# Optimization experiments

Measured on AMD Instinct MI355X. Metric: run time of the kernel, lower is better.

Reference implementation:

```python
import jax, jax.numpy as jnp
import numpy as np

N, G = 10000, 200          # nodes, graphs
EL, EG = 160000, 500000    # local / global edges
S, V = 256, 64             # scalar / vector hidden dims
NA, NB = 16, 5             # atom types, bond types


def _lin(k, i, o):
    return (jax.random.normal(k, (i, o), jnp.float32) / np.sqrt(i))


def scatter_mean(vals, idx, num_segments):
    # vals: [N, ...]; idx: [N] int
    sums = jax.ops.segment_sum(vals, idx, num_segments=num_segments)
    cnt = jax.ops.segment_sum(jnp.ones((vals.shape[0],), vals.dtype), idx,
                              num_segments=num_segments)
    cnt = jnp.maximum(cnt, 1.0).reshape((-1,) + (1,) * (vals.ndim - 1))
    return sums / cnt


def calc_edge_attrs(edge_index, pos):
    src, tgt = edge_index[0], edge_index[1]
    r = pos[tgt] - pos[src]                      # [E,3]
    a = (pos[tgt] * pos[src]).sum(-1)            # [E]
    d = jnp.sqrt(jnp.clip((r ** 2).sum(-1), 1e-6))
    r_norm = r / d[:, None]
    return d, a, r_norm


def setup_inputs() -> dict:
    key = jax.random.key(0)
    ks = jax.random.split(key, 24)
    inp = {}
    inp["x"] = jax.random.normal(ks[0], (N, NA), jnp.float32)
    inp["t"] = jax.random.uniform(ks[1], (G, 1), jnp.float32)
    inp["pos"] = jax.random.normal(ks[2], (N, 3), jnp.float32)
    eil = jax.random.randint(ks[3], (2, EL), 0, N)
    eig = jax.random.randint(ks[4], (2, EG), 0, N)
    # avoid self-edges so edge distances are strictly positive (safe sqrt grads)
    eig = eig.at[1].set(jnp.where(eig[1] == eig[0], (eig[1] + 1) % N, eig[1]))
    eil = eil.at[1].set(jnp.where(eil[1] == eil[0], (eil[1] + 1) % N, eil[1]))
    inp["edge_index_local"] = eil
    inp["edge_index_global"] = eig
    inp["edge_attr_global"] = jax.random.normal(ks[5], (EG, NB), jnp.float32)
    inp["batch"] = jnp.sort(jax.random.randint(ks[6], (N,), 0, G))
    # learned parameters
    inp["W_time"], inp["b_time"] = _lin(ks[7], 1, S), jnp.zeros((S,), jnp.float32)
    inp["W_atom"], inp["b_atom"] = _lin(ks[8], NA, S), jnp.zeros((S,), jnp.float32)
    inp["W_at"], inp["b_at"] = _lin(ks[9], S, S), jnp.zeros((S,), jnp.float32)
    inp["W_shared"], inp["b_shared"] = _lin(ks[10], S, S), jnp.zeros((S,), jnp.float32)
    inp["W_b0"], inp["b_b0"] = _lin(ks[11], S + 1, S), jnp.zeros((S,), jnp.float32)
    inp["W_b1"], inp["b_b1"] = _lin(ks[12], S, 2 * NB), jnp.zeros((2 * NB,), jnp.float32)
    inp["W_coord"] = _lin(ks[13], V, 2)           # no bias
    inp["W_atoms"], inp["b_atoms"] = _lin(ks[14], S, 2 * NA), jnp.zeros((2 * NA,), jnp.float32)
    return inp


def reference(x, t, pos, edge_attr_global, W_time, b_time, W_atom, b_atom,
              W_at, b_at, W_shared, b_shared, W_b0, b_b0, W_b1, b_b1,
              W_coord, W_atoms, b_atoms,
              edge_index_local, edge_index_global, batch):
    # --- trunk: center positions, embed atoms + time ---
    pos = pos - scatter_mean(pos, batch, G)[batch]
    temb = t @ W_time + b_time                    # [G,S]
    tnode = temb[batch]                           # [N,S]
    s = x @ W_atom + b_atom
    s = (s + tnode) @ W_at + b_at                 # [N,S]
    # --- edge attrs (gather-compute pattern feeding the GNN) ---
    d_l, a_l, rn_l = calc_edge_attrs(edge_index_local, pos)
    d_g, a_g, rn_g = calc_edge_attrs(edge_index_global, pos)
    # GNN stand-in (identity on s, v, p): v initialized to zeros as in original
    v = jnp.zeros((N, 3, V), s.dtype)
    # --- prediction head ---
    s = jax.nn.silu(s @ W_shared + b_shared)
    j, i = edge_index_global[0], edge_index_global[1]
    d = jnp.sqrt(((pos[i] - pos[j]) ** 2).sum(-1, keepdims=True))  # [EG,1]
    edge = jnp.concatenate([s[i] + s[j], d], axis=-1)              # [EG,S+1]
    bonds = jax.nn.silu(edge @ W_b0 + b_b0) @ W_b1 + b_b1          # [EG,2*NB]
    bonds_pred, bonds_eps = bonds[:, :NB], bonds[:, NB:]
    coords = jnp.einsum('nkv,vo->nko', v, W_coord)                 # [N,3,2]
    coords = coords - scatter_mean(coords, batch, G)[batch]
    coords_eps0, coords_eps1 = coords[..., 0], coords[..., 1]      # [N,3]
    atoms = s @ W_atoms + b_atoms                                  # [N,2*NA]
    atoms_eps, atoms_pred = atoms[:, :NA], atoms[:, NA:]
    pos_c = pos - scatter_mean(pos, batch, G)[batch]
    coords_pred = pos_c + coords_eps1
    return (coords_pred, coords_eps0, atoms_pred, atoms_eps,
            bonds_pred, bonds_eps, d_l, rn_l, a_g, rn_g)
```

## Files before the change

kernel.cpp:

```cpp
#include <hip/hip_runtime.h>
#include <hip/hip_bf16.h>

typedef __hip_bfloat16 bf16;
typedef short bf16x8 __attribute__((ext_vector_type(8)));
typedef float f32x4 __attribute__((ext_vector_type(4)));
typedef float f32x2 __attribute__((ext_vector_type(2)));
typedef _Float16 f16x2 __attribute__((ext_vector_type(2)));
typedef _Float16 f16x8 __attribute__((ext_vector_type(8)));
typedef __fp16 fp16x2 __attribute__((ext_vector_type(2)));

#define N_NODES  10000
#define G_GRAPHS 200
#define EL_EDGES 160000
#define EG_EDGES 500000
#define S_DIM    256
#define APAD     264

#define BONDS2        7813
#define LOCAL_BLOCKS  625

#define WS_FLAG   0
#define WS_POSC   1024
#define WS_WDH    31232
#define WS_W1F    31488
#define WS_BB0R   33536
#define WS_BB1    34304
#define WS_WATOM  34560
#define WS_WTIME  38656
#define WS_BTIME  38912
#define WS_BATOM  39168
#define WS_BAT    39424
#define WS_BSH    39680
#define WS_BATOMS 39936
#define WS_T      40000
#define WS_X      40448
#define WT_AT     200448
#define WT_SH     233216
#define WT_B0     265984
#define WT_ATOMS  298752
#define WS_H      303968
#define WS_END_FLOATS 944224

#define CHAN(S)    ((((S) >> 6) << 6) + (((S) & 3) << 4) + (((S) & 63) >> 2))

#define O_CPRED 0
#define O_CEPS  30000
#define O_APRED 60000
#define O_AEPS  220000
#define O_BPRED 380000
#define O_BEPS  2880000
#define O_DL    5380000
#define O_RNL   5540000
#define O_AG    6020000
#define O_RNG   6520000

__device__ __forceinline__ float b2f(bf16 v) { return __bfloat162float(v); }
__device__ __forceinline__ bf16  f2b(float v) { return __float2bfloat16(v); }
__device__ __forceinline__ unsigned short bbits(float v) {
    bf16 b = f2b(v);
    return *reinterpret_cast<unsigned short*>(&b);
}
__device__ __forceinline__ unsigned short h16bits(float v) {
    _Float16 h = (_Float16)v;
    return *reinterpret_cast<unsigned short*>(&h);
}
__device__ __forceinline__ float ldin(const void* p, int idx, int isf32) {
    return isf32 ? ((const float*)p)[idx] : b2f(((const bf16*)p)[idx]);
}
__device__ __forceinline__ void stout(void* out, int f32o, size_t idx, float v) {
    if (f32o) ((float*)out)[idx] = v;
    else      ((bf16*)out)[idx]  = f2b(v);
}
__device__ __forceinline__ float silu(float p) {
    return p * __builtin_amdgcn_rcpf(1.0f + __expf(-p));
}
__device__ __forceinline__ _Float16 h_exp2(_Float16 x) {
    _Float16 r;
    asm("v_exp_f16 %0, %1" : "=v"(r) : "v"(x));
    return r;
}
__device__ __forceinline__ _Float16 h_rcp(_Float16 x) {
    _Float16 r;
    asm("v_rcp_f16 %0, %1" : "=v"(r) : "v"(x));
    return r;
}
__device__ __forceinline__ f16x2 hsilu2(f16x2 p) {
    const _Float16 nl = (_Float16)(-1.44269504f);
    f16x2 q = p * (f16x2){nl, nl};
    f16x2 ex;
    ex[0] = h_exp2(q[0]);
    ex[1] = h_exp2(q[1]);
    f16x2 den = ex + (f16x2){(_Float16)1.0f, (_Float16)1.0f};
    f16x2 rc;
    rc[0] = h_rcp(den[0]);
    rc[1] = h_rcp(den[1]);
    return p * rc;
}
template<bool HI>
__device__ __forceinline__ f16x2 dec2(int enc) {
    f32x2 f = __builtin_amdgcn_cvt_pk_f32_fp8(enc, HI);
    union { fp16x2 a; f16x2 b; } u;
    u.a = __builtin_amdgcn_cvt_pkrtz(f[0], f[1]);
    return u.b;
}
__device__ __forceinline__ int dtype_f32(const void* tt) {
    const unsigned short* q = (const unsigned short*)tt;
    int c = 0;
#pragma unroll
    for (int z = 0; z < 32; ++z) c += (q[z] >= 0x4000) ? 1 : 0;
    return c > 0;
}

__global__ void k_prep(const void* __restrict__ x, const void* __restrict__ tt,
                       const void* __restrict__ W_time, const void* __restrict__ b_time,
                       const void* __restrict__ W_atom, const void* __restrict__ b_atom,
                       const void* __restrict__ W_at, const void* __restrict__ b_at,
                       const void* __restrict__ W_shared, const void* __restrict__ b_shared,
                       const void* __restrict__ W_b0, const void* __restrict__ b_b0,
                       const void* __restrict__ W_b1, const void* __restrict__ b_b1,
                       const void* __restrict__ W_atoms, const void* __restrict__ b_atoms,
                       float* __restrict__ ws) {
    const int t = blockIdx.x * blockDim.x + threadIdx.x;
    const int f = dtype_f32(tt);
    if (t == 0) ws[WS_FLAG] = f ? 1.0f : 0.0f;
    if (t < 65536) {
        const int k = t >> 8, n = t & 255;
        ((unsigned short*)(ws + WT_AT))[n * 256 + k] = bbits(ldin(W_at, t, f));
        ((unsigned short*)(ws + WT_SH))[n * 256 + k] = bbits(ldin(W_shared, t, f));
        ((unsigned short*)(ws + WT_B0))[n * 256 + k] = bbits(ldin(W_b0, t, f));
    }
    if (t < 160000) ws[WS_X + t] = ldin(x, t, f);
    if (t < 8192) {
        const int k = t >> 5, n = t & 31;
        ((unsigned short*)(ws + WT_ATOMS))[n * 256 + k] = bbits(ldin(W_atoms, t, f));
    }
    if (t < 4096) {
        const int i = t & 7, lc = (t >> 3) & 15, q = (t >> 7) & 3, ts = t >> 9;
        const int s = ts * 32 + q * 8 + i;
        float v = (lc < 10) ? ldin(W_b1, CHAN(s) * 10 + lc, f) : 0.0f;
        ((unsigned short*)(ws + WS_W1F))[t] = h16bits(v);
    }
    if (t < 4096) ws[WS_WATOM + t] = ldin(W_atom, t, f);
    if (t < 256) {
        ((unsigned short*)(ws + WS_WDH))[t] = h16bits(ldin(W_b0, 65536 + CHAN(t), f));
        ws[WS_BB0R + t] = ldin(b_b0, t, f);
        ws[WS_WTIME + t] = ldin(W_time, t, f);
        ws[WS_BTIME + t] = ldin(b_time, t, f);
        ws[WS_BATOM + t] = ldin(b_atom, t, f);
        ws[WS_BAT + t]   = ldin(b_at, t, f);
        ws[WS_BSH + t]   = ldin(b_shared, t, f);
    }
    if (t < 200) ws[WS_T + t] = ldin(tt, t, f);
    if (t < 32)  ws[WS_BATOMS + t] = ldin(b_atoms, t, f);
    if (t < 16)  ws[WS_BB1 + t] = (t < 10) ? ldin(b_b1, t, f) : 0.0f;
}

__global__ void k_pos(const void* __restrict__ pos, const int* __restrict__ batch,
                      float* __restrict__ ws, void* __restrict__ out) {
    const int g = blockIdx.x;
    const int f32o = ws[WS_FLAG] != 0.0f;
    __shared__ int s_lo, s_hi;
    __shared__ float wsum[4][3];
    __shared__ float mean[3];
    if (threadIdx.x == 0) {
        int lo = 0, hi = N_NODES;
        while (lo < hi) { int m = (lo + hi) >> 1; if (batch[m] < g) lo = m + 1; else hi = m; }
        s_lo = lo;
        int lo2 = lo; hi = N_NODES;
        while (lo2 < hi) { int m = (lo2 + hi) >> 1; if (batch[m] < g + 1) lo2 = m + 1; else hi = m; }
        s_hi = lo2;
    }
    __syncthreads();
    const int lo = s_lo, hi = s_hi, cnt = hi - lo;
    float sx = 0.f, sy = 0.f, sz = 0.f;
    for (int n = lo + threadIdx.x; n < hi; n += 256) {
        sx += ldin(pos, n * 3 + 0, f32o);
        sy += ldin(pos, n * 3 + 1, f32o);
        sz += ldin(pos, n * 3 + 2, f32o);
    }
#pragma unroll
    for (int off = 32; off > 0; off >>= 1) {
        sx += __shfl_down(sx, off);
        sy += __shfl_down(sy, off);
        sz += __shfl_down(sz, off);
    }
    if ((threadIdx.x & 63) == 0) {
        wsum[threadIdx.x >> 6][0] = sx;
        wsum[threadIdx.x >> 6][1] = sy;
        wsum[threadIdx.x >> 6][2] = sz;
    }
    __syncthreads();
    if (threadIdx.x == 0) {
        float inv = 1.0f / (float)max(cnt, 1);
        mean[0] = (wsum[0][0] + wsum[1][0] + wsum[2][0] + wsum[3][0]) * inv;
        mean[1] = (wsum[0][1] + wsum[1][1] + wsum[2][1] + wsum[3][1]) * inv;
        mean[2] = (wsum[0][2] + wsum[1][2] + wsum[2][2] + wsum[3][2]) * inv;
    }
    __syncthreads();
    for (int n = lo + threadIdx.x; n < hi; n += 256) {
#pragma unroll
        for (int k = 0; k < 3; ++k) {
            float p = ldin(pos, n * 3 + k, f32o) - mean[k];
            ws[WS_POSC + n * 3 + k] = p;
            stout(out, f32o, O_CPRED + n * 3 + k, p);
            stout(out, f32o, O_CEPS + n * 3 + k, 0.0f);
        }
    }
}

__global__ __launch_bounds__(256) void k_node(
    const int* __restrict__ batch, const float* __restrict__ ws,
    unsigned int* __restrict__ h_out, void* __restrict__ out) {
    __shared__ unsigned short actA[16][APAD];
    __shared__ unsigned short actB[16][APAD];
    const int tid = threadIdx.x;
    const int wave = tid >> 6, lane = tid & 63;
    const int quad = lane >> 4, l16 = lane & 15;
    const int row0 = blockIdx.x * 16;

    {
        const int r = tid >> 4;
        const int c0 = (tid & 15) * 16;
        const int g = row0 + r;
        float tb = ws[WS_T + batch[g]];
        float xr[16];
#pragma unroll
        for (int k = 0; k < 16; ++k) xr[k] = ws[WS_X + g * 16 + k];
        for (int cc = 0; cc < 16; cc += 4) {
            const int c = c0 + cc;
            float a0 = ws[WS_BATOM + c + 0] + tb * ws[WS_WTIME + c + 0] + ws[WS_BTIME + c + 0];
            float a1 = ws[WS_BATOM + c + 1] + tb * ws[WS_WTIME + c + 1] + ws[WS_BTIME + c + 1];
            float a2 = ws[WS_BATOM + c + 2] + tb * ws[WS_WTIME + c + 2] + ws[WS_BTIME + c + 2];
            float a3 = ws[WS_BATOM + c + 3] + tb * ws[WS_WTIME + c + 3] + ws[WS_BTIME + c + 3];
#pragma unroll
            for (int k = 0; k < 16; ++k) {
                float4 w4 = *(const float4*)(ws + WS_WATOM + k * S_DIM + c);
                a0 += xr[k] * w4.x; a1 += xr[k] * w4.y;
                a2 += xr[k] * w4.z; a3 += xr[k] * w4.w;
            }
            actA[r][c + 0] = bbits(a0); actA[r][c + 1] = bbits(a1);
            actA[r][c + 2] = bbits(a2); actA[r][c + 3] = bbits(a3);
        }
    }
    __syncthreads();

    const unsigned short* wt_at = (const unsigned short*)(ws + WT_AT);
    const unsigned short* wt_sh = (const unsigned short*)(ws + WT_SH);
    const unsigned short* wt_b0 = (const unsigned short*)(ws + WT_B0);
    const unsigned short* wt_am = (const unsigned short*)(ws + WT_ATOMS);
    const int n0 = wave * 64;

    {
        f32x4 acc[4] = {};
        for (int kk = 0; kk < S_DIM; kk += 32) {
            const int k = kk + quad * 8;
            bf16x8 a = *(const bf16x8*)&actA[l16][k];
#pragma unroll
            for (int nt = 0; nt < 4; ++nt) {
                bf16x8 b = *(const bf16x8*)(wt_at + (size_t)(n0 + nt * 16 + l16) * S_DIM + k);
                acc[nt] = __builtin_amdgcn_mfma_f32_16x16x32_bf16(a, b, acc[nt], 0, 0, 0);
            }
        }
#pragma unroll
        for (int nt = 0; nt < 4; ++nt) {
            const int n = n0 + nt * 16 + l16;
            const float bv = ws[WS_BAT + n];
#pragma unroll
            for (int r = 0; r < 4; ++r)
                actB[quad * 4 + r][n] = bbits(acc[nt][r] + bv);
        }
    }
    __syncthreads();

    {
        f32x4 acc[4] = {};
        for (int kk = 0; kk < S_DIM; kk += 32) {
            const int k = kk + quad * 8;
            bf16x8 a = *(const bf16x8*)&actB[l16][k];
#pragma unroll
            for (int nt = 0; nt < 4; ++nt) {
                bf16x8 b = *(const bf16x8*)(wt_sh + (size_t)(n0 + nt * 16 + l16) * S_DIM + k);
                acc[nt] = __builtin_amdgcn_mfma_f32_16x16x32_bf16(a, b, acc[nt], 0, 0, 0);
            }
        }
        __syncthreads();
#pragma unroll
        for (int nt = 0; nt < 4; ++nt) {
            const int n = n0 + nt * 16 + l16;
            const float bv = ws[WS_BSH + n];
#pragma unroll
            for (int r = 0; r < 4; ++r)
                actA[quad * 4 + r][n] = bbits(silu(acc[nt][r] + bv));
        }
    }
    __syncthreads();

    {
        f32x4 acc[4] = {};
        for (int kk = 0; kk < S_DIM; kk += 32) {
            const int k = kk + quad * 8;
            bf16x8 a = *(const bf16x8*)&actA[l16][k];
#pragma unroll
            for (int nt = 0; nt < 4; ++nt) {
                bf16x8 b = *(const bf16x8*)(wt_b0 + (size_t)(n0 + nt * 16 + l16) * S_DIM + k);
                acc[nt] = __builtin_amdgcn_mfma_f32_16x16x32_bf16(a, b, acc[nt], 0, 0, 0);
            }
        }
        float bh[4];
#pragma unroll
        for (int nt = 0; nt < 4; ++nt) bh[nt] = 0.5f * ws[WS_BB0R + n0 + nt * 16 + l16];
#pragma unroll
        for (int r = 0; r < 4; ++r) {
            const int g = row0 + quad * 4 + r;
            int w = 0;
            w = __builtin_amdgcn_cvt_pk_fp8_f32(acc[0][r] + bh[0], acc[1][r] + bh[1], w, false);
            w = __builtin_amdgcn_cvt_pk_fp8_f32(acc[2][r] + bh[2], acc[3][r] + bh[3], w, true);
            h_out[(size_t)g * 64 + wave * 16 + l16] = (unsigned int)w;
        }
    }

    if (wave < 2) {
        f32x4 acc = {};
        const int n = wave * 16 + l16;
        for (int kk = 0; kk < S_DIM; kk += 32) {
            const int k = kk + quad * 8;
            bf16x8 a = *(const bf16x8*)&actA[l16][k];
            bf16x8 b = *(const bf16x8*)(wt_am + (size_t)n * S_DIM + k);
            acc = __builtin_amdgcn_mfma_f32_16x16x32_bf16(a, b, acc, 0, 0, 0);
        }
        const float bv = ws[WS_BATOMS + n];
        const int f32o = ws[WS_FLAG] != 0.0f;
#pragma unroll
        for (int r = 0; r < 4; ++r) {
            const int g = row0 + quad * 4 + r;
            float v = acc[r] + bv;
            if (n < 16) stout(out, f32o, O_AEPS + (size_t)g * 16 + n, v);
            else        stout(out, f32o, O_APRED + (size_t)g * 16 + (n - 16), v);
        }
    }
}

union U8 { f16x8 v; f16x2 p[4]; };

__global__ __launch_bounds__(256, 4) void k_edges(const int* __restrict__ eig,
                                                  const int* __restrict__ eil,
                                                  const float* __restrict__ ws,
                                                  const unsigned char* __restrict__ h,
                                                  void* __restrict__ out) {
    __shared__ unsigned char sm[4][32][256];
    const int f32o = ws[WS_FLAG] != 0.0f;

    if (blockIdx.x >= BONDS2) {
        const int e = (blockIdx.x - BONDS2) * 256 + threadIdx.x;
        const float* posc = ws + WS_POSC;
        const int s = eil[e];
        const int t = eil[EL_EDGES + e];
        float rx = posc[t * 3 + 0] - posc[s * 3 + 0];
        float ry = posc[t * 3 + 1] - posc[s * 3 + 1];
        float rz = posc[t * 3 + 2] - posc[s * 3 + 2];
        float dsq = rx * rx + ry * ry + rz * rz;
        float d = sqrtf(fmaxf(dsq, 1e-6f));
        float inv = 1.0f / d;
        stout(out, f32o, O_DL + e, d);
        stout(out, f32o, O_RNL + (size_t)e * 3 + 0, rx * inv);
        stout(out, f32o, O_RNL + (size_t)e * 3 + 1, ry * inv);
        stout(out, f32o, O_RNL + (size_t)e * 3 + 2, rz * inv);
        return;
    }

    const int wave = threadIdx.x >> 6, lane = threadIdx.x & 63;
    const int quad = lane >> 4, l16 = lane & 15;
    const int e0 = blockIdx.x * 64 + wave * 16;
    if (e0 >= EG_EDGES) return;

    unsigned char* smw = &sm[wave][0][0];

#pragma unroll
    for (int p = 0; p < 8; ++p) {
        const int r16 = (p & 3) * 4 + quad;
        const int es = e0 + r16;
        const int node = (p < 4) ? eig[EG_EDGES + es]
                                 : eig[es];
        const int row = (p < 4) ? r16 : 16 + r16;
        uint4 v = *(const uint4*)(h + (size_t)node * 256 + l16 * 16);
        *(uint4*)(smw + row * 256 + ((l16 ^ (r16 >> 1)) << 4)) = v;
    }

    const int e = e0 + l16;
    const int j = eig[e];
    const int i = eig[EG_EDGES + e];
    const float* posc = ws + WS_POSC;
    float pix = posc[i * 3 + 0], piy = posc[i * 3 + 1], piz = posc[i * 3 + 2];
    float pjx = posc[j * 3 + 0], pjy = posc[j * 3 + 1], pjz = posc[j * 3 + 2];
    float rx = pix - pjx, ry = piy - pjy, rz = piz - pjz;
    float dsq = rx * rx + ry * ry + rz * rz;
    float dgeo = sqrtf(dsq);
    if (quad == 0) {
        float ag = pix * pjx + piy * pjy + piz * pjz;
        float inv = 1.0f / sqrtf(fmaxf(dsq, 1e-6f));
        stout(out, f32o, O_AG + e, ag);
        stout(out, f32o, O_RNG + (size_t)e * 3 + 0, rx * inv);
        stout(out, f32o, O_RNG + (size_t)e * 3 + 1, ry * inv);
        stout(out, f32o, O_RNG + (size_t)e * 3 + 2, rz * inv);
    }

    const _Float16 hd = (_Float16)dgeo;
    const f16x2 d2h = {hd, hd};
    const unsigned short* wdh = (const unsigned short*)(ws + WS_WDH);
    const _Float16* w1f = (const _Float16*)(ws + WS_W1F) + (quad * 16 + l16) * 8;
    const int r2 = l16 >> 1;
    const unsigned char* rowA = smw + l16 * 256;
    const unsigned char* rowB = smw + (16 + l16) * 256;

    f32x4 acc = {};
#pragma unroll 2
    for (int t = 0; t < 8; ++t) {
        const int off = (((2 * t + (quad >> 1)) ^ r2) << 4) + ((quad & 1) << 3);
        uint2 ua = *(const uint2*)(rowA + off);
        uint2 ub = *(const uint2*)(rowB + off);
        U8 W;  W.v = *(const f16x8*)(wdh + t * 32 + quad * 8);
        f16x8 WF = *(const f16x8*)(w1f + t * 512);
        f16x2 s0 = dec2<false>((int)ua.x) + dec2<false>((int)ub.x);
        f16x2 s1 = dec2<true>((int)ua.x)  + dec2<true>((int)ub.x);
        f16x2 s2 = dec2<false>((int)ua.y) + dec2<false>((int)ub.y);
        f16x2 s3 = dec2<true>((int)ua.y)  + dec2<true>((int)ub.y);
        U8 U;
        U.p[0] = hsilu2(s0 + d2h * W.p[0]);
        U.p[1] = hsilu2(s1 + d2h * W.p[1]);
        U.p[2] = hsilu2(s2 + d2h * W.p[2]);
        U.p[3] = hsilu2(s3 + d2h * W.p[3]);
        acc = __builtin_amdgcn_mfma_f32_16x16x32_f16(U.v, WF, acc, 0, 0, 0);
    }

    if (l16 < 10) {
        const float bv = ws[WS_BB1 + l16];
#pragma unroll
        for (int r = 0; r < 4; ++r) {
            const int er = e0 + quad * 4 + r;
            float v = acc[r] + bv;
            if (l16 < 5) stout(out, f32o, O_BPRED + (size_t)er * 5 + l16, v);
            else         stout(out, f32o, O_BEPS + (size_t)er * 5 + (l16 - 5), v);
        }
    }
}

extern "C" void kernel_launch(void* const* d_in, const int* in_sizes, int n_in,
                              void* d_out, int out_size, void* d_ws, size_t ws_size,
                              hipStream_t stream) {
    const void* x        = d_in[0];
    const void* t        = d_in[1];
    const void* pos      = d_in[2];
    const int*  eil      = (const int*)d_in[3];
    const int*  eig      = (const int*)d_in[4];
    const int*  batch    = (const int*)d_in[6];
    const void* W_time   = d_in[7];
    const void* b_time   = d_in[8];
    const void* W_atom   = d_in[9];
    const void* b_atom   = d_in[10];
    const void* W_at     = d_in[11];
    const void* b_at     = d_in[12];
    const void* W_shared = d_in[13];
    const void* b_shared = d_in[14];
    const void* W_b0     = d_in[15];
    const void* b_b0     = d_in[16];
    const void* W_b1     = d_in[17];
    const void* b_b1     = d_in[18];
    const void* W_atoms  = d_in[20];
    const void* b_atoms  = d_in[21];
    (void)in_sizes; (void)n_in; (void)out_size;

    const size_t NEED = (size_t)WS_END_FLOATS * sizeof(float);
    if (ws_size < NEED) return;

    float* ws = (float*)d_ws;
    unsigned int* hbuf = (unsigned int*)(ws + WS_H);

    k_prep<<<640, 256, 0, stream>>>(x, t, W_time, b_time, W_atom, b_atom,
                                    W_at, b_at, W_shared, b_shared, W_b0, b_b0,
                                    W_b1, b_b1, W_atoms, b_atoms, ws);
    k_pos<<<G_GRAPHS, 256, 0, stream>>>(pos, batch, ws, d_out);
    k_node<<<N_NODES / 16, 256, 0, stream>>>(batch, ws, hbuf, d_out);
    k_edges<<<BONDS2 + LOCAL_BLOCKS, 256, 0, stream>>>(
        eig, eil, ws, (const unsigned char*)hbuf, d_out);
}
```

Before: 229.6 us.

## Split bond-edge K dimension across wave pairs and use direct fp8-to-f16 convert

Each 16-edge tile is now processed by two waves that each handle half of the 256-wide hidden dimension, and their partial MFMA accumulators are combined through shared memory after a block barrier. Per-wave LDS shrinks to half, grid size doubles, and launch bounds raise the occupancy target, all to hide gather latency with more parallelism. The fp8 decode uses a single scaled pk_f16_fp8 conversion where the builtin is available, skipping the f32 intermediate. The cost is an extra __syncthreads, an LDS reduction, and duplicated index and position loads per edge.

Result: no change. 225.7 us (-1.7%).

```diff
diff --git a/kernel.cpp b/kernel.cpp
--- a/kernel.cpp
+++ b/kernel.cpp
@@ -16,7 +16,7 @@
 #define S_DIM    256
 #define APAD     264
 
-#define BONDS2        7813
+#define BONDS3        15625
 #define LOCAL_BLOCKS  625
 
 #define WS_FLAG   0
@@ -96,12 +96,22 @@
     rc[1] = h_rcp(den[1]);
     return p * rc;
 }
+#if defined(__has_builtin)
+#if __has_builtin(__builtin_amdgcn_cvt_scalef32_pk_f16_fp8)
+#define HAVE_SCALEF16 1
+#endif
+#endif
 template<bool HI>
 __device__ __forceinline__ f16x2 dec2(int enc) {
+#ifdef HAVE_SCALEF16
+    auto r = __builtin_amdgcn_cvt_scalef32_pk_f16_fp8((unsigned int)enc, 1.0f, HI);
+    return __builtin_bit_cast(f16x2, r);
+#else
     f32x2 f = __builtin_amdgcn_cvt_pk_f32_fp8(enc, HI);
     union { fp16x2 a; f16x2 b; } u;
     u.a = __builtin_amdgcn_cvt_pkrtz(f[0], f[1]);
     return u.b;
+#endif
 }
 __device__ __forceinline__ int dtype_f32(const void* tt) {
     const unsigned short* q = (const unsigned short*)tt;
@@ -342,16 +352,16 @@
 
 union U8 { f16x8 v; f16x2 p[4]; };
 
-__global__ __launch_bounds__(256, 4) void k_edges(const int* __restrict__ eig,
+__global__ __launch_bounds__(256, 8) void k_edges(const int* __restrict__ eig,
                                                   const int* __restrict__ eil,
                                                   const float* __restrict__ ws,
                                                   const unsigned char* __restrict__ h,
                                                   void* __restrict__ out) {
-    __shared__ unsigned char sm[4][32][256];
+    __shared__ __align__(16) unsigned char sm[4][32][128];
     const int f32o = ws[WS_FLAG] != 0.0f;
 
-    if (blockIdx.x >= BONDS2) {
-        const int e = (blockIdx.x - BONDS2) * 256 + threadIdx.x;
+    if (blockIdx.x >= BONDS3) {
+        const int e = (blockIdx.x - BONDS3) * 256 + threadIdx.x;
         const float* posc = ws + WS_POSC;
         const int s = eil[e];
         const int t = eil[EL_EDGES + e];
@@ -370,20 +380,20 @@
 
     const int wave = threadIdx.x >> 6, lane = threadIdx.x & 63;
     const int quad = lane >> 4, l16 = lane & 15;
-    const int e0 = blockIdx.x * 64 + wave * 16;
-    if (e0 >= EG_EDGES) return;
-
+    const int P = wave >> 1, sub = wave & 1;
+    const int e0 = blockIdx.x * 32 + P * 16;
     unsigned char* smw = &sm[wave][0][0];
 
-#pragma unroll
-    for (int p = 0; p < 8; ++p) {
-        const int r16 = (p & 3) * 4 + quad;
+    const int l8 = lane & 7, rg = lane >> 3;
+#pragma unroll
+    for (int p = 0; p < 4; ++p) {
+        const int row = p * 8 + rg;
+        const int r16 = row & 15;
         const int es = e0 + r16;
-        const int node = (p < 4) ? eig[EG_EDGES + es]
-                                 : eig[es];
-        const int row = (p < 4) ? r16 : 16 + r16;
-        uint4 v = *(const uint4*)(h + (size_t)node * 256 + l16 * 16);
-        *(uint4*)(smw + row * 256 + ((l16 ^ (r16 >> 1)) << 4)) = v;
+        const int node = (row < 16) ? eig[EG_EDGES + es]
+                                    : eig[es];
+        uint4 v = *(const uint4*)(h + (size_t)node * 256 + sub * 128 + l8 * 16);
+        *(uint4*)(smw + row * 128 + ((l8 ^ (row & 7)) << 4)) = v;
     }
 
     const int e = e0 + l16;
@@ -395,7 +405,7 @@
     float rx = pix - pjx, ry = piy - pjy, rz = piz - pjz;
     float dsq = rx * rx + ry * ry + rz * rz;
     float dgeo = sqrtf(dsq);
-    if (quad == 0) {
+    if (sub == 0 && quad == 0) {
         float ag = pix * pjx + piy * pjy + piz * pjz;
         float inv = 1.0f / sqrtf(fmaxf(dsq, 1e-6f));
         stout(out, f32o, O_AG + e, ag);
@@ -406,16 +416,17 @@
 
     const _Float16 hd = (_Float16)dgeo;
     const f16x2 d2h = {hd, hd};
-    const unsigned short* wdh = (const unsigned short*)(ws + WS_WDH);
-    const _Float16* w1f = (const _Float16*)(ws + WS_W1F) + (quad * 16 + l16) * 8;
-    const int r2 = l16 >> 1;
-    const unsigned char* rowA = smw + l16 * 256;
-    const unsigned char* rowB = smw + (16 + l16) * 256;
+    const unsigned short* wdh = (const unsigned short*)(ws + WS_WDH) + sub * 128;
+    const _Float16* w1f = (const _Float16*)(ws + WS_W1F)
+                        + (size_t)(sub * 4) * 512 + (quad * 16 + l16) * 8;
+    const int rx7 = l16 & 7;
+    const unsigned char* rowA = smw + l16 * 128;
+    const unsigned char* rowB = smw + (16 + l16) * 128;
 
     f32x4 acc = {};
-#pragma unroll 2
-    for (int t = 0; t < 8; ++t) {
-        const int off = (((2 * t + (quad >> 1)) ^ r2) << 4) + ((quad & 1) << 3);
+#pragma unroll
+    for (int t = 0; t < 4; ++t) {
+        const int off = (((2 * t + (quad >> 1)) ^ rx7) << 4) + ((quad & 1) << 3);
         uint2 ua = *(const uint2*)(rowA + off);
         uint2 ub = *(const uint2*)(rowB + off);
         U8 W;  W.v = *(const f16x8*)(wdh + t * 32 + quad * 8);
@@ -432,12 +443,15 @@
         acc = __builtin_amdgcn_mfma_f32_16x16x32_f16(U.v, WF, acc, 0, 0, 0);
     }
 
-    if (l16 < 10) {
+    if (sub == 1) ((f32x4*)smw)[lane] = acc;
+    __syncthreads();
+    if (sub == 0 && l16 < 10) {
+        f32x4 o = ((f32x4*)(smw + 4096))[lane];
         const float bv = ws[WS_BB1 + l16];
 #pragma unroll
         for (int r = 0; r < 4; ++r) {
             const int er = e0 + quad * 4 + r;
-            float v = acc[r] + bv;
+            float v = acc[r] + o[r] + bv;
             if (l16 < 5) stout(out, f32o, O_BPRED + (size_t)er * 5 + l16, v);
             else         stout(out, f32o, O_BEPS + (size_t)er * 5 + (l16 - 5), v);
         }
@@ -480,6 +494,6 @@
                                     W_b1, b_b1, W_atoms, b_atoms, ws);
     k_pos<<<G_GRAPHS, 256, 0, stream>>>(pos, batch, ws, d_out);
     k_node<<<N_NODES / 16, 256, 0, stream>>>(batch, ws, hbuf, d_out);
-    k_edges<<<BONDS2 + LOCAL_BLOCKS, 256, 0, stream>>>(
+    k_edges<<<BONDS3 + LOCAL_BLOCKS, 256, 0, stream>>>(
         eig, eil, ws, (const unsigned char*)hbuf, d_out);
 }
```
